# Kernel optimization log

Measured on AMD Instinct MI355X. Metric: run time of the kernel, lower is better.

The kernel has to match this reference:

```python
import jax, jax.numpy as jnp
import numpy as np

T, H, E, I = 1024, 2048, 8, 5632  # tokens, hidden, experts, intermediate


def setup_inputs() -> dict:
    key = jax.random.key(0)
    k1, k2, k3, k4 = jax.random.split(key, 4)
    return {
        "hidden_states": jax.random.normal(k1, (T, H), dtype=jnp.float32),
        "router_logits": jax.random.normal(k2, (T, E), dtype=jnp.float32),
        "w13_weight": jax.random.normal(k3, (E, 2 * I, H), dtype=jnp.float32) * 0.02,
        "w2_weight": jax.random.normal(k4, (E, H, I), dtype=jnp.float32) * 0.02,
        "top_k": 2,
    }


def reference(hidden_states, router_logits, w13_weight, w2_weight, top_k):
    # --- routing: softmax (fp32) + top-k + renormalize, as in fused_moe ---
    probs = jax.nn.softmax(router_logits.astype(jnp.float32), axis=-1)  # [T,E]
    topk_w, topk_idx = jax.lax.top_k(probs, top_k)                      # [T,k]
    topk_w = topk_w / jnp.sum(topk_w, axis=-1, keepdims=True)           # renormalize
    # combine weights scattered to dense [T,E] (zero for unselected experts)
    one_hot = jax.nn.one_hot(topk_idx, probs.shape[-1], dtype=topk_w.dtype)  # [T,k,E]
    combine = jnp.einsum('tk,tke->te', topk_w, one_hot)                 # [T,E]

    # --- expert MLP: SiLU(x @ w1^T) * (x @ w3^T) @ w2^T ---
    h13 = jnp.einsum('th,eih->eti', hidden_states, w13_weight)          # [E,T,2I]
    inter = w13_weight.shape[1] // 2
    gate, up = h13[:, :, :inter], h13[:, :, inter:]
    act = jax.nn.silu(gate) * up                                        # [E,T,I]
    out_e = jnp.einsum('eti,ehi->eth', act, w2_weight)                  # [E,T,H]

    # --- weighted combine over selected experts ---
    out = jnp.einsum('eth,te->th', out_e, combine.astype(out_e.dtype))  # [T,H]
    return out
```

## Files before the change

### kernel.cpp

```cpp
#include <hip/hip_runtime.h>
#include <stdint.h>

#define T_TOK 1024
#define HID   2048
#define NE    8
#define INTER 5632
#define I2    11264
#define BK    64
#define MAXT  18
#define RMAX  2560
#define KCH   2816

typedef __bf16 bf16x8 __attribute__((ext_vector_type(8)));
typedef __bf16 bf16x4 __attribute__((ext_vector_type(4)));
typedef float  f32x4  __attribute__((ext_vector_type(4)));
typedef unsigned short u16;
typedef u16 u16x8 __attribute__((ext_vector_type(8)));


__device__ __forceinline__ int swz(int row, int cb) {
    return row * 128 + (cb ^ ((row & 7) << 4));
}

__device__ __forceinline__ bf16x4 cvt4(float4 v) {
    bf16x4 r;
    r[0] = (__bf16)v.x; r[1] = (__bf16)v.y; r[2] = (__bf16)v.z; r[3] = (__bf16)v.w;
    return r;
}

__global__ __launch_bounds__(256) void moe_pack(const float* __restrict__ h,
                                                u16* __restrict__ hpk) {
    int i = blockIdx.x * blockDim.x + threadIdx.x;
    float4 a = ((const float4*)h)[2 * i];
    float4 b = ((const float4*)h)[2 * i + 1];
    bf16x8 o;
    o[0] = (__bf16)a.x; o[1] = (__bf16)a.y; o[2] = (__bf16)a.z; o[3] = (__bf16)a.w;
    o[4] = (__bf16)b.x; o[5] = (__bf16)b.y; o[6] = (__bf16)b.z; o[7] = (__bf16)b.w;
    ((bf16x8*)hpk)[i] = o;
}

__global__ void moe_router(const float* __restrict__ logits,
                           int* __restrict__ mi, float* __restrict__ mf) {
    int t = blockIdx.x * blockDim.x + threadIdx.x;
    if (t >= T_TOK) return;
    float l[NE];
#pragma unroll
    for (int i = 0; i < NE; ++i) l[i] = logits[t * NE + i];
    int e0 = 0; float v0 = l[0];
#pragma unroll
    for (int i = 1; i < NE; ++i) if (l[i] > v0) { v0 = l[i]; e0 = i; }
    int e1 = -1; float v1 = -3.4e38f;
#pragma unroll
    for (int i = 0; i < NE; ++i) if (i != e0 && l[i] > v1) { v1 = l[i]; e1 = i; }
    float ex = __expf(v1 - v0);
    float s  = 1.f + ex;
    mi[256 + 2 * t]     = e0;
    mi[256 + 2 * t + 1] = e1;
    mf[8192 + 2 * t]     = 1.f / s;
    mf[8192 + 2 * t + 1] = ex / s;
    atomicAdd(&mi[e0], 1);
    atomicAdd(&mi[e1], 1);
}

__global__ void moe_plan(int* __restrict__ mi) {
    int tid = threadIdx.x;
    if (tid == 0) {
        int off = 0, nt = 0;
        for (int e = 0; e < NE; ++e) {
            int c = mi[e];
            mi[24 + e] = off;
            int c64 = ((c + 63) >> 6) << 6;
            int ntile = (c64 + 255) >> 8;
            for (int j = 0; j < ntile; ++j) {
                mi[32 + 2 * nt]     = e;
                mi[32 + 2 * nt + 1] = off + j * 256;
                ++nt;
            }
            off += c64;
            mi[8 + e] = 0;
        }
        mi[16] = nt;
    }
    for (int i = tid; i < RMAX; i += blockDim.x) mi[2560 + i] = -1;
}

__global__ void moe_scatter(int* __restrict__ mi, float* __restrict__ mf) {
    int t = blockIdx.x * blockDim.x + threadIdx.x;
    if (t >= T_TOK) return;
    int e0 = mi[256 + 2 * t], e1 = mi[256 + 2 * t + 1];
    float w0 = mf[8192 + 2 * t], w1 = mf[8192 + 2 * t + 1];
    int p0 = atomicAdd(&mi[8 + e0], 1);
    int s0 = mi[24 + e0] + p0;
    mi[2560 + s0] = t; mf[5632 + s0] = w0;
    int p1 = atomicAdd(&mi[8 + e1], 1);
    int s1 = mi[24 + e1] + p1;
    mi[2560 + s1] = t; mf[5632 + s1] = w1;
}


#define G1_LOAD(K0)                                                          \
    _Pragma("unroll")                                                        \
    for (int it = 0; it < 4; ++it) {                                         \
        u16x8 z = {};                                                        \
        raa[it] = ap1[it] ? *(const u16x8*)(ap1[it] + (K0)) : z;             \
    }                                                                        \
    _Pragma("unroll")                                                        \
    for (int it = 0; it < 2; ++it) {                                         \
        rg[it] = *(const float4*)(bgp[it] + (K0));                           \
        ru[it] = *(const float4*)(bup[it] + (K0));                           \
    }

#define G1_WRITE()                                                           \
    _Pragma("unroll")                                                        \
    for (int it = 0; it < 4; ++it)                                           \
        *(u16x8*)(As + swz((tid >> 3) + it * 64, acb)) = raa[it];            \
    _Pragma("unroll")                                                        \
    for (int it = 0; it < 2; ++it) {                                         \
        *(bf16x4*)(Bgs + swz(sr + it * 32, scb)) = cvt4(rg[it]);             \
        *(bf16x4*)(Bus + swz(sr + it * 32, scb)) = cvt4(ru[it]);             \
    }

#define G1_MFMA()                                                            \
    _Pragma("unroll")                                                        \
    for (int kk = 0; kk < 2; ++kk) {                                         \
        int kb = kk * 64 + lk * 16;                                          \
        bf16x8 a0 = *(const bf16x8*)(As + swz(w * 32 + lrow, kb));           \
        bf16x8 a1 = *(const bf16x8*)(As + swz(w * 32 + 16 + lrow, kb));      \
        _Pragma("unroll")                                                    \
        for (int fn = 0; fn < 4; ++fn) {                                     \
            bf16x8 bg = *(const bf16x8*)(Bgs + swz(fn * 16 + lrow, kb));     \
            bf16x8 bu = *(const bf16x8*)(Bus + swz(fn * 16 + lrow, kb));     \
            accg[0][fn] = __builtin_amdgcn_mfma_f32_16x16x32_bf16(a0, bg, accg[0][fn], 0, 0, 0); \
            accg[1][fn] = __builtin_amdgcn_mfma_f32_16x16x32_bf16(a1, bg, accg[1][fn], 0, 0, 0); \
            accu[0][fn] = __builtin_amdgcn_mfma_f32_16x16x32_bf16(a0, bu, accu[0][fn], 0, 0, 0); \
            accu[1][fn] = __builtin_amdgcn_mfma_f32_16x16x32_bf16(a1, bu, accu[1][fn], 0, 0, 0); \
        }                                                                    \
    }

__global__ __launch_bounds__(512) void moe_gemm1(
        const u16* __restrict__ hpk, const float* __restrict__ w13,
        const int* __restrict__ mi, u16* __restrict__ act) {
    const int bid = blockIdx.x;
    const int s   = (bid & 7) * 198 + (bid >> 3);
    const int tj  = s % MAXT;
    const int ct  = s / MAXT;
    if (tj >= mi[16]) return;
    const int e = mi[32 + 2 * tj], row_base = mi[32 + 2 * tj + 1];
    const int* rowtok = mi + 2560;
    const int limit = mi[24 + e] + (((mi[e] + 63) >> 6) << 6);

    __shared__ __align__(16) char smem[50176];
    char* As  = smem;
    char* Bgs = smem + 32768;
    char* Bus = smem + 40960;
    int*  toks = (int*)(smem + 49152);

    const int tid = threadIdx.x;
    const int w = tid >> 6, lane = tid & 63;
    const int lrow = lane & 15, lk = lane >> 4;

    const int sr  = tid >> 4;
    const int sc  = (tid & 15) * 4;
    const int scb = (tid & 15) * 8;
    const int acb = (tid & 7) * 16;

    if (tid < 256) {
        int idx = row_base + tid;
        toks[tid] = (idx < limit) ? rowtok[idx] : -1;
    }
    __syncthreads();

    const u16* ap1[4];
#pragma unroll
    for (int it = 0; it < 4; ++it) {
        int tok = toks[(tid >> 3) + it * 64];
        ap1[it] = (tok >= 0) ? hpk + (size_t)tok * HID + (tid & 7) * 8 : nullptr;
    }
    const float* bg_base = w13 + ((size_t)e * I2 + (size_t)ct * 64) * HID;
    const float* bu_base = bg_base + (size_t)INTER * HID;
    const float* bgp[2];
    const float* bup[2];
#pragma unroll
    for (int it = 0; it < 2; ++it) {
        bgp[it] = bg_base + (size_t)(sr + it * 32) * HID + sc;
        bup[it] = bu_base + (size_t)(sr + it * 32) * HID + sc;
    }

    f32x4 accg[2][4] = {}, accu[2][4] = {};
    u16x8 raa[4]; float4 rg[2], ru[2];

    G1_LOAD(0)
    G1_WRITE()
    __syncthreads();
    for (int k0 = BK; k0 <= HID; k0 += BK) {
        const bool more = k0 < HID;
        if (more) { G1_LOAD(k0) }
        G1_MFMA()
        __syncthreads();
        if (more) { G1_WRITE() __syncthreads(); }
    }

    const size_t actbase = (size_t)row_base * INTER + (size_t)ct * 64;
#pragma unroll
    for (int fm = 0; fm < 2; ++fm)
#pragma unroll
    for (int fn = 0; fn < 4; ++fn)
#pragma unroll
    for (int j = 0; j < 4; ++j) {
        int row = w * 32 + fm * 16 + lk * 4 + j;
        int col = fn * 16 + lrow;
        if (toks[row] >= 0) {
            float g = accg[fm][fn][j], u = accu[fm][fn][j];
            float a = g / (1.f + __expf(-g)) * u;
            ((__bf16*)act)[actbase + (size_t)row * INTER + col] = (__bf16)a;
        }
    }
}


#define G2_LOAD(K0)                                                          \
    _Pragma("unroll")                                                        \
    for (int it = 0; it < 4; ++it) {                                         \
        u16x8 z = {};                                                        \
        raa[it] = ap2[it] ? *(const u16x8*)(ap2[it] + (K0)) : z;             \
    }                                                                        \
    _Pragma("unroll")                                                        \
    for (int it = 0; it < 2; ++it)                                           \
        rb[it] = *(const float4*)(bp2[it] + (K0));

#define G2_WRITE()                                                           \
    _Pragma("unroll")                                                        \
    for (int it = 0; it < 4; ++it)                                           \
        *(u16x8*)(As2 + swz((tid >> 3) + it * 64, acb)) = raa[it];           \
    _Pragma("unroll")                                                        \
    for (int it = 0; it < 2; ++it)                                           \
        *(bf16x4*)(Bs2 + swz(sr + it * 32, scb)) = cvt4(rb[it]);

#define G2_MFMA()                                                            \
    _Pragma("unroll")                                                        \
    for (int kk = 0; kk < 2; ++kk) {                                         \
        int kb = kk * 64 + lk * 16;                                          \
        bf16x8 a0 = *(const bf16x8*)(As2 + swz(w * 32 + lrow, kb));          \
        bf16x8 a1 = *(const bf16x8*)(As2 + swz(w * 32 + 16 + lrow, kb));     \
        _Pragma("unroll")                                                    \
        for (int fn = 0; fn < 4; ++fn) {                                     \
            bf16x8 b = *(const bf16x8*)(Bs2 + swz(fn * 16 + lrow, kb));      \
            acc[0][fn] = __builtin_amdgcn_mfma_f32_16x16x32_bf16(a0, b, acc[0][fn], 0, 0, 0); \
            acc[1][fn] = __builtin_amdgcn_mfma_f32_16x16x32_bf16(a1, b, acc[1][fn], 0, 0, 0); \
        }                                                                    \
    }

__global__ __launch_bounds__(512) void moe_gemm2(
        const u16* __restrict__ act, const float* __restrict__ w2,
        const int* __restrict__ mi, const float* __restrict__ mf,
        float* __restrict__ out) {
    const int bid = blockIdx.x;
    const int s   = (bid & 7) * 144 + (bid >> 3);
    const int tj  = s % MAXT;
    const int ct  = (s / MAXT) % 32;
    const int kz  = s / (MAXT * 32);
    if (tj >= mi[16]) return;
    const int e = mi[32 + 2 * tj], row_base = mi[32 + 2 * tj + 1];
    const int* rowtok = mi + 2560;
    const float* roww = mf + 5632;
    const int limit = mi[24 + e] + (((mi[e] + 63) >> 6) << 6);

    __shared__ __align__(16) char smem[40960];
    char* As2 = smem;
    char* Bs2 = smem + 32768;

    const int tid = threadIdx.x;
    const int w = tid >> 6, lane = tid & 63;
    const int lrow = lane & 15, lk = lane >> 4;

    const int sr  = tid >> 4;
    const int sc  = (tid & 15) * 4;
    const int scb = (tid & 15) * 8;
    const int ac  = (tid & 7) * 8;
    const int acb = (tid & 7) * 16;
    const int kbeg = kz * KCH, kend = kbeg + KCH;

    const u16* ap2[4];
#pragma unroll
    for (int it = 0; it < 4; ++it) {
        int slot = row_base + (tid >> 3) + it * 64;
        bool ok = (slot < limit) && (rowtok[slot] >= 0);
        ap2[it] = ok ? act + (size_t)slot * INTER + ac : nullptr;
    }
    const float* b_base = w2 + ((size_t)e * HID + (size_t)ct * 64) * INTER;
    const float* bp2[2];
#pragma unroll
    for (int it = 0; it < 2; ++it)
        bp2[it] = b_base + (size_t)(sr + it * 32) * INTER + sc;

    f32x4 acc[2][4] = {};
    u16x8 raa[4]; float4 rb[2];

    G2_LOAD(kbeg)
    G2_WRITE()
    __syncthreads();
    for (int k0 = kbeg + BK; k0 <= kend; k0 += BK) {
        const bool more = k0 < kend;
        if (more) { G2_LOAD(k0) }
        G2_MFMA()
        __syncthreads();
        if (more) { G2_WRITE() __syncthreads(); }
    }

#pragma unroll
    for (int fm = 0; fm < 2; ++fm)
#pragma unroll
    for (int fn = 0; fn < 4; ++fn)
#pragma unroll
    for (int j = 0; j < 4; ++j) {
        int row = w * 32 + fm * 16 + lk * 4 + j;
        int col = fn * 16 + lrow;
        int slot = row_base + row;
        if (slot < limit) {
            int tok = rowtok[slot];
            if (tok >= 0)
                atomicAdd(out + (size_t)tok * HID + (size_t)ct * 64 + col,
                          acc[fm][fn][j] * roww[slot]);
        }
    }
}

extern "C" void kernel_launch(void* const* d_in, const int* in_sizes, int n_in,
                              void* d_out, int out_size, void* d_ws, size_t ws_size,
                              hipStream_t stream) {
    const float* hidden = (const float*)d_in[0];
    const float* logits = (const float*)d_in[1];
    const float* w13    = (const float*)d_in[2];
    const float* w2     = (const float*)d_in[3];
    float* out = (float*)d_out;

    int*   mi  = (int*)d_ws;
    float* mf  = (float*)d_ws;
    u16*   act = (u16*)((char*)d_ws + 65536);
    u16*   hpk = (u16*)((char*)d_ws + 33554432);

    hipMemsetAsync(d_ws, 0, 64, stream);
    hipMemsetAsync(d_out, 0, (size_t)out_size * sizeof(float), stream);

    moe_pack<<<dim3(T_TOK * HID / 8 / 256), 256, 0, stream>>>(hidden, hpk);
    moe_router<<<dim3(T_TOK / 256), 256, 0, stream>>>(logits, mi, mf);
    moe_plan<<<dim3(1), 256, 0, stream>>>(mi);
    moe_scatter<<<dim3(T_TOK / 256), 256, 0, stream>>>(mi, mf);
    moe_gemm1<<<dim3(MAXT * (INTER / 64)), 512, 0, stream>>>(hpk, w13, mi, act);
    moe_gemm2<<<dim3(MAXT * (HID / 64) * 2), 512, 0, stream>>>(act, w2, mi, mf, out);
}
```

Baseline: 507.9 us.

## Widen MoE GEMM tiles to 128 columns with 1024-thread blocks

Both expert GEMMs now use 1024-thread blocks laid out as an 8x2 wave grid, so each block covers 128 output columns instead of 64 over the same 256-row token tile. The wider tile halves the number of blocks and halves the redundant reloads of activation rows per weight column. The cost is more LDS per block (66 KB for gemm1), likely only one block per CU, and fewer blocks to spread across the GPU, which may reduce latency hiding.

```diff
diff --git a/kernel.cpp b/kernel.cpp
--- a/kernel.cpp
+++ b/kernel.cpp
@@ -100,7 +100,7 @@
 
 #define G1_LOAD(K0)                                                          \
     _Pragma("unroll")                                                        \
-    for (int it = 0; it < 4; ++it) {                                         \
+    for (int it = 0; it < 2; ++it) {                                         \
         u16x8 z = {};                                                        \
         raa[it] = ap1[it] ? *(const u16x8*)(ap1[it] + (K0)) : z;             \
     }                                                                        \
@@ -112,24 +112,24 @@
 
 #define G1_WRITE()                                                           \
     _Pragma("unroll")                                                        \
-    for (int it = 0; it < 4; ++it)                                           \
-        *(u16x8*)(As + swz((tid >> 3) + it * 64, acb)) = raa[it];            \
+    for (int it = 0; it < 2; ++it)                                           \
+        *(u16x8*)(As + swz((tid >> 3) + it * 128, acb)) = raa[it];           \
     _Pragma("unroll")                                                        \
     for (int it = 0; it < 2; ++it) {                                         \
-        *(bf16x4*)(Bgs + swz(sr + it * 32, scb)) = cvt4(rg[it]);             \
-        *(bf16x4*)(Bus + swz(sr + it * 32, scb)) = cvt4(ru[it]);             \
+        *(bf16x4*)(Bgs + swz((tid >> 4) + it * 64, scb)) = cvt4(rg[it]);     \
+        *(bf16x4*)(Bus + swz((tid >> 4) + it * 64, scb)) = cvt4(ru[it]);     \
     }
 
 #define G1_MFMA()                                                            \
     _Pragma("unroll")                                                        \
     for (int kk = 0; kk < 2; ++kk) {                                         \
         int kb = kk * 64 + lk * 16;                                          \
-        bf16x8 a0 = *(const bf16x8*)(As + swz(w * 32 + lrow, kb));           \
-        bf16x8 a1 = *(const bf16x8*)(As + swz(w * 32 + 16 + lrow, kb));      \
+        bf16x8 a0 = *(const bf16x8*)(As + swz(wm * 32 + lrow, kb));          \
+        bf16x8 a1 = *(const bf16x8*)(As + swz(wm * 32 + 16 + lrow, kb));     \
         _Pragma("unroll")                                                    \
         for (int fn = 0; fn < 4; ++fn) {                                     \
-            bf16x8 bg = *(const bf16x8*)(Bgs + swz(fn * 16 + lrow, kb));     \
-            bf16x8 bu = *(const bf16x8*)(Bus + swz(fn * 16 + lrow, kb));     \
+            bf16x8 bg = *(const bf16x8*)(Bgs + swz(wn * 64 + fn * 16 + lrow, kb)); \
+            bf16x8 bu = *(const bf16x8*)(Bus + swz(wn * 64 + fn * 16 + lrow, kb)); \
             accg[0][fn] = __builtin_amdgcn_mfma_f32_16x16x32_bf16(a0, bg, accg[0][fn], 0, 0, 0); \
             accg[1][fn] = __builtin_amdgcn_mfma_f32_16x16x32_bf16(a1, bg, accg[1][fn], 0, 0, 0); \
             accu[0][fn] = __builtin_amdgcn_mfma_f32_16x16x32_bf16(a0, bu, accu[0][fn], 0, 0, 0); \
@@ -137,11 +137,11 @@
         }                                                                    \
     }
 
-__global__ __launch_bounds__(512) void moe_gemm1(
+__global__ __launch_bounds__(1024) void moe_gemm1(
         const u16* __restrict__ hpk, const float* __restrict__ w13,
         const int* __restrict__ mi, u16* __restrict__ act) {
     const int bid = blockIdx.x;
-    const int s   = (bid & 7) * 198 + (bid >> 3);
+    const int s   = (bid & 7) * 99 + (bid >> 3);
     const int tj  = s % MAXT;
     const int ct  = s / MAXT;
     if (tj >= mi[16]) return;
@@ -149,17 +149,17 @@
     const int* rowtok = mi + 2560;
     const int limit = mi[24 + e] + (((mi[e] + 63) >> 6) << 6);
 
-    __shared__ __align__(16) char smem[50176];
+    __shared__ __align__(16) char smem[66560];
     char* As  = smem;
     char* Bgs = smem + 32768;
-    char* Bus = smem + 40960;
-    int*  toks = (int*)(smem + 49152);
+    char* Bus = smem + 49152;
+    int*  toks = (int*)(smem + 65536);
 
     const int tid = threadIdx.x;
     const int w = tid >> 6, lane = tid & 63;
+    const int wm = w >> 1, wn = w & 1;
     const int lrow = lane & 15, lk = lane >> 4;
 
-    const int sr  = tid >> 4;
     const int sc  = (tid & 15) * 4;
     const int scb = (tid & 15) * 8;
     const int acb = (tid & 7) * 16;
@@ -170,24 +170,24 @@
     }
     __syncthreads();
 
-    const u16* ap1[4];
-#pragma unroll
-    for (int it = 0; it < 4; ++it) {
-        int tok = toks[(tid >> 3) + it * 64];
+    const u16* ap1[2];
+#pragma unroll
+    for (int it = 0; it < 2; ++it) {
+        int tok = toks[(tid >> 3) + it * 128];
         ap1[it] = (tok >= 0) ? hpk + (size_t)tok * HID + (tid & 7) * 8 : nullptr;
     }
-    const float* bg_base = w13 + ((size_t)e * I2 + (size_t)ct * 64) * HID;
+    const float* bg_base = w13 + ((size_t)e * I2 + (size_t)ct * 128) * HID;
     const float* bu_base = bg_base + (size_t)INTER * HID;
     const float* bgp[2];
     const float* bup[2];
 #pragma unroll
     for (int it = 0; it < 2; ++it) {
-        bgp[it] = bg_base + (size_t)(sr + it * 32) * HID + sc;
-        bup[it] = bu_base + (size_t)(sr + it * 32) * HID + sc;
+        bgp[it] = bg_base + (size_t)((tid >> 4) + it * 64) * HID + sc;
+        bup[it] = bu_base + (size_t)((tid >> 4) + it * 64) * HID + sc;
     }
 
     f32x4 accg[2][4] = {}, accu[2][4] = {};
-    u16x8 raa[4]; float4 rg[2], ru[2];
+    u16x8 raa[2]; float4 rg[2], ru[2];
 
     G1_LOAD(0)
     G1_WRITE()
@@ -200,15 +200,15 @@
         if (more) { G1_WRITE() __syncthreads(); }
     }
 
-    const size_t actbase = (size_t)row_base * INTER + (size_t)ct * 64;
+    const size_t actbase = (size_t)row_base * INTER + (size_t)ct * 128;
 #pragma unroll
     for (int fm = 0; fm < 2; ++fm)
 #pragma unroll
     for (int fn = 0; fn < 4; ++fn)
 #pragma unroll
     for (int j = 0; j < 4; ++j) {
-        int row = w * 32 + fm * 16 + lk * 4 + j;
-        int col = fn * 16 + lrow;
+        int row = wm * 32 + fm * 16 + lk * 4 + j;
+        int col = wn * 64 + fn * 16 + lrow;
         if (toks[row] >= 0) {
             float g = accg[fm][fn][j], u = accu[fm][fn][j];
             float a = g / (1.f + __expf(-g)) * u;
@@ -220,7 +220,7 @@
 
 #define G2_LOAD(K0)                                                          \
     _Pragma("unroll")                                                        \
-    for (int it = 0; it < 4; ++it) {                                         \
+    for (int it = 0; it < 2; ++it) {                                         \
         u16x8 z = {};                                                        \
         raa[it] = ap2[it] ? *(const u16x8*)(ap2[it] + (K0)) : z;             \
     }                                                                        \
@@ -230,71 +230,71 @@
 
 #define G2_WRITE()                                                           \
     _Pragma("unroll")                                                        \
-    for (int it = 0; it < 4; ++it)                                           \
-        *(u16x8*)(As2 + swz((tid >> 3) + it * 64, acb)) = raa[it];           \
-    _Pragma("unroll")                                                        \
     for (int it = 0; it < 2; ++it)                                           \
-        *(bf16x4*)(Bs2 + swz(sr + it * 32, scb)) = cvt4(rb[it]);
+        *(u16x8*)(As2 + swz((tid >> 3) + it * 128, acb)) = raa[it];          \
+    _Pragma("unroll")                                                        \
+    for (int it = 0; it < 2; ++it)                                           \
+        *(bf16x4*)(Bs2 + swz((tid >> 4) + it * 64, scb)) = cvt4(rb[it]);
 
 #define G2_MFMA()                                                            \
     _Pragma("unroll")                                                        \
     for (int kk = 0; kk < 2; ++kk) {                                         \
         int kb = kk * 64 + lk * 16;                                          \
-        bf16x8 a0 = *(const bf16x8*)(As2 + swz(w * 32 + lrow, kb));          \
-        bf16x8 a1 = *(const bf16x8*)(As2 + swz(w * 32 + 16 + lrow, kb));     \
+        bf16x8 a0 = *(const bf16x8*)(As2 + swz(wm * 32 + lrow, kb));         \
+        bf16x8 a1 = *(const bf16x8*)(As2 + swz(wm * 32 + 16 + lrow, kb));    \
         _Pragma("unroll")                                                    \
         for (int fn = 0; fn < 4; ++fn) {                                     \
-            bf16x8 b = *(const bf16x8*)(Bs2 + swz(fn * 16 + lrow, kb));      \
+            bf16x8 b = *(const bf16x8*)(Bs2 + swz(wn * 64 + fn * 16 + lrow, kb)); \
             acc[0][fn] = __builtin_amdgcn_mfma_f32_16x16x32_bf16(a0, b, acc[0][fn], 0, 0, 0); \
             acc[1][fn] = __builtin_amdgcn_mfma_f32_16x16x32_bf16(a1, b, acc[1][fn], 0, 0, 0); \
         }                                                                    \
     }
 
-__global__ __launch_bounds__(512) void moe_gemm2(
+__global__ __launch_bounds__(1024) void moe_gemm2(
         const u16* __restrict__ act, const float* __restrict__ w2,
         const int* __restrict__ mi, const float* __restrict__ mf,
         float* __restrict__ out) {
     const int bid = blockIdx.x;
-    const int s   = (bid & 7) * 144 + (bid >> 3);
+    const int s   = (bid & 7) * 72 + (bid >> 3);
     const int tj  = s % MAXT;
-    const int ct  = (s / MAXT) % 32;
-    const int kz  = s / (MAXT * 32);
+    const int ct  = (s / MAXT) % 16;
+    const int kz  = s / (MAXT * 16);
     if (tj >= mi[16]) return;
     const int e = mi[32 + 2 * tj], row_base = mi[32 + 2 * tj + 1];
     const int* rowtok = mi + 2560;
     const float* roww = mf + 5632;
     const int limit = mi[24 + e] + (((mi[e] + 63) >> 6) << 6);
 
-    __shared__ __align__(16) char smem[40960];
+    __shared__ __align__(16) char smem[49152];
     char* As2 = smem;
     char* Bs2 = smem + 32768;
 
     const int tid = threadIdx.x;
     const int w = tid >> 6, lane = tid & 63;
+    const int wm = w >> 1, wn = w & 1;
     const int lrow = lane & 15, lk = lane >> 4;
 
-    const int sr  = tid >> 4;
     const int sc  = (tid & 15) * 4;
     const int scb = (tid & 15) * 8;
     const int ac  = (tid & 7) * 8;
     const int acb = (tid & 7) * 16;
     const int kbeg = kz * KCH, kend = kbeg + KCH;
 
-    const u16* ap2[4];
-#pragma unroll
-    for (int it = 0; it < 4; ++it) {
-        int slot = row_base + (tid >> 3) + it * 64;
+    const u16* ap2[2];
+#pragma unroll
+    for (int it = 0; it < 2; ++it) {
+        int slot = row_base + (tid >> 3) + it * 128;
         bool ok = (slot < limit) && (rowtok[slot] >= 0);
         ap2[it] = ok ? act + (size_t)slot * INTER + ac : nullptr;
     }
-    const float* b_base = w2 + ((size_t)e * HID + (size_t)ct * 64) * INTER;
+    const float* b_base = w2 + ((size_t)e * HID + (size_t)ct * 128) * INTER;
     const float* bp2[2];
 #pragma unroll
     for (int it = 0; it < 2; ++it)
-        bp2[it] = b_base + (size_t)(sr + it * 32) * INTER + sc;
+        bp2[it] = b_base + (size_t)((tid >> 4) + it * 64) * INTER + sc;
 
     f32x4 acc[2][4] = {};
-    u16x8 raa[4]; float4 rb[2];
+    u16x8 raa[2]; float4 rb[2];
 
     G2_LOAD(kbeg)
     G2_WRITE()
@@ -313,13 +313,13 @@
     for (int fn = 0; fn < 4; ++fn)
 #pragma unroll
     for (int j = 0; j < 4; ++j) {
-        int row = w * 32 + fm * 16 + lk * 4 + j;
-        int col = fn * 16 + lrow;
+        int row = wm * 32 + fm * 16 + lk * 4 + j;
+        int col = wn * 64 + fn * 16 + lrow;
         int slot = row_base + row;
         if (slot < limit) {
             int tok = rowtok[slot];
             if (tok >= 0)
-                atomicAdd(out + (size_t)tok * HID + (size_t)ct * 64 + col,
+                atomicAdd(out + (size_t)tok * HID + (size_t)ct * 128 + col,
                           acc[fm][fn][j] * roww[slot]);
         }
     }
@@ -346,6 +346,6 @@
     moe_router<<<dim3(T_TOK / 256), 256, 0, stream>>>(logits, mi, mf);
     moe_plan<<<dim3(1), 256, 0, stream>>>(mi);
     moe_scatter<<<dim3(T_TOK / 256), 256, 0, stream>>>(mi, mf);
-    moe_gemm1<<<dim3(MAXT * (INTER / 64)), 512, 0, stream>>>(hpk, w13, mi, act);
-    moe_gemm2<<<dim3(MAXT * (HID / 64) * 2), 512, 0, stream>>>(act, w2, mi, mf, out);
-}
+    moe_gemm1<<<dim3(MAXT * (INTER / 128)), 1024, 0, stream>>>(hpk, w13, mi, act);
+    moe_gemm2<<<dim3(MAXT * (HID / 128) * 2), 1024, 0, stream>>>(act, w2, mi, mf, out);
+}
```

Result: faster. 494.0 us (-2.7%).
